# Performance work log

Measured on AMD Instinct MI355X. Metric: run time of the kernel, lower is better.

The kernel has to match this reference:

```python
import jax, jax.numpy as jnp
import numpy as np

N, E, IN, OUT, T = 50000, 800000, 16, 16, 8
LN_EPS = 1e-5


def setup_inputs() -> dict:
    key = jax.random.key(0)
    ks = jax.random.split(key, 8)
    x = jax.random.normal(ks[0], (N, IN), dtype=jnp.float32)
    edge_index = jax.random.randint(ks[1], (2, E), 0, N, dtype=jnp.int64)
    edge_attr = jax.random.normal(ks[2], (E, T), dtype=jnp.float32)
    # LayerNorm params
    ln_gamma = jnp.ones((IN,), dtype=jnp.float32)
    ln_beta = jnp.zeros((IN,), dtype=jnp.float32)
    # edge_nn: Linear(t, in*out)
    w_edge = jax.random.normal(ks[3], (T, IN * OUT), dtype=jnp.float32) * (1.0 / np.sqrt(T))
    b_edge = jax.random.normal(ks[4], (IN * OUT,), dtype=jnp.float32) * 0.01
    # NNConv root weight [in, out] and bias [out]
    root = jax.random.normal(ks[5], (IN, OUT), dtype=jnp.float32) * (1.0 / np.sqrt(IN))
    bias = jax.random.normal(ks[6], (OUT,), dtype=jnp.float32) * 0.01
    return {"x": x, "edge_index": edge_index, "edge_attr": edge_attr,
            "ln_gamma": ln_gamma, "ln_beta": ln_beta,
            "w_edge": w_edge, "b_edge": b_edge, "root": root, "bias": bias}


def reference(x, edge_index, edge_attr, ln_gamma, ln_beta, w_edge, b_edge, root, bias):
    # pre: LayerNorm -> ReLU (Dropout is identity in eval mode)
    mu = jnp.mean(x, axis=-1, keepdims=True)
    var = jnp.mean((x - mu) ** 2, axis=-1, keepdims=True)
    h = (x - mu) * jax.lax.rsqrt(var + LN_EPS) * ln_gamma + ln_beta
    h = jax.nn.relu(h)  # [N, IN]

    # edge MLP -> per-edge weight matrices [E, IN, OUT]
    theta = (edge_attr @ w_edge + b_edge).reshape(E, IN, OUT)

    src = edge_index[0]  # message source j
    dst = edge_index[1]  # aggregation target i (PyG source_to_target flow)

    # per-edge matmul: x_j [E, IN] x theta [E, IN, OUT] -> [E, OUT]
    msg = jnp.einsum('ei,eio->eo', h[src], theta)

    # scatter-add into target nodes
    agg = jax.ops.segment_sum(msg, dst, num_segments=N)  # [N, OUT]

    # root transform + bias
    out = agg + h @ root + bias
    return out
```

## Files before the change

### kernel.cpp

```cpp
#include <hip/hip_runtime.h>

#define N_NODES 50000
#define E_EDGES 800000
#define NTILES  (E_EDGES / 16)

typedef __attribute__((ext_vector_type(8))) short short8;
typedef __attribute__((ext_vector_type(4))) float floatx4;

__device__ __forceinline__ short f2bf(float x) {
    union { float f; unsigned u; } v; v.f = x;
    unsigned r = v.u + 0x7FFFu + ((v.u >> 16) & 1u);
    return (short)(r >> 16);
}

__device__ __forceinline__ unsigned pk_bf16(float lo, float hi) {
    union { float f; unsigned u; } a, b; a.f = lo; b.f = hi;
    return __builtin_amdgcn_perm(b.u, a.u, 0x07060302u);
}

__global__ __launch_bounds__(256) void node_kernel(
    const float* __restrict__ x, const float* __restrict__ gamma,
    const float* __restrict__ beta, const float* __restrict__ root,
    const float* __restrict__ bias, float* __restrict__ h,
    float* __restrict__ out)
{
    int n = blockIdx.x * blockDim.x + threadIdx.x;
    if (n >= N_NODES) return;
    const float* xr = x + n * 16;
    float xv[16];
    #pragma unroll
    for (int i = 0; i < 4; ++i) ((floatx4*)xv)[i] = ((const floatx4*)xr)[i];
    float mu = 0.f;
    #pragma unroll
    for (int i = 0; i < 16; ++i) mu += xv[i];
    mu *= (1.f / 16.f);
    float var = 0.f;
    #pragma unroll
    for (int i = 0; i < 16; ++i) { float d = xv[i] - mu; var += d * d; }
    var *= (1.f / 16.f);
    float rs = rsqrtf(var + 1e-5f);
    float hv[16];
    #pragma unroll
    for (int i = 0; i < 16; ++i) {
        float t = (xv[i] - mu) * rs * gamma[i] + beta[i];
        hv[i] = t > 0.f ? t : 0.f;
    }
    float* hr = h + n * 16;
    #pragma unroll
    for (int i = 0; i < 4; ++i) ((floatx4*)hr)[i] = ((floatx4*)hv)[i];
    float ov[16];
    #pragma unroll
    for (int o = 0; o < 16; ++o) ov[o] = bias[o];
    #pragma unroll
    for (int i = 0; i < 16; ++i) {
        float hi = hv[i];
        #pragma unroll
        for (int o = 0; o < 16; ++o) ov[o] += hi * root[i * 16 + o];
    }
    float* orow = out + n * 16;
    #pragma unroll
    for (int i = 0; i < 4; ++i) ((floatx4*)orow)[i] = ((floatx4*)ov)[i];
}

__global__ __launch_bounds__(256) void prep_kernel(
    const float* __restrict__ w_edge, const float* __restrict__ b_edge,
    short* __restrict__ w2t)
{
    int t = blockIdx.x * blockDim.x + threadIdx.x;
    if (t >= 16 * 160) return;
    int m = t / 160, k = t % 160;
    float v = 0.f;
    if (k < 128)      v = w_edge[(k >> 4) * 256 + (k & 15) * 16 + m];
    else if (k < 144) v = b_edge[(k - 128) * 16 + m];
    w2t[m * 160 + k] = f2bf(v);
}

__global__ __launch_bounds__(256) void edge_kernel(
    const int* __restrict__ eidx, const float* __restrict__ ea,
    const short* __restrict__ w2t, const float* __restrict__ h,
    float* __restrict__ out)
{
    const int lane = threadIdx.x & 63;
    const int wid  = threadIdx.x >> 6;
    const int m = lane & 15;
    const int q = lane >> 4;

    const int tile = blockIdx.x * 4 + wid;
    if (tile >= NTILES) return;

    const int e   = tile * 16 + m;
    const int src = eidx[e];
    const int dst = eidx[E_EDGES + e];

    const short* wp = w2t + m * 160 + 8 * q;
    short8 bfrag[5];
    #pragma unroll
    for (int c = 0; c < 5; ++c)
        bfrag[c] = *(const short8*)(wp + 32 * c);

    const float* er = ea + (size_t)e * 8;
    floatx4 ea0 = ((const floatx4*)er)[0];
    floatx4 ea1 = ((const floatx4*)er)[1];

    const float* hr = h + src * 16 + 8 * (q & 1);
    floatx4 h0 = ((const floatx4*)hr)[0];
    floatx4 h1 = ((const floatx4*)hr)[1];
    float hh[8] = {h0.x, h0.y, h0.z, h0.w, h1.x, h1.y, h1.z, h1.w};

    floatx4 acc = {0.f, 0.f, 0.f, 0.f};
    const int hi_t = q >> 1;
    #pragma unroll
    for (int c = 0; c < 4; ++c) {
        float t_even, t_odd;
        if (c == 0)      { t_even = ea0.x; t_odd = ea0.y; }
        else if (c == 1) { t_even = ea0.z; t_odd = ea0.w; }
        else if (c == 2) { t_even = ea1.x; t_odd = ea1.y; }
        else             { t_even = ea1.z; t_odd = ea1.w; }
        float s = hi_t ? t_odd : t_even;
        union { short8 s8; unsigned u[4]; } af;
        #pragma unroll
        for (int p = 0; p < 4; ++p)
            af.u[p] = pk_bf16(s * hh[2 * p], s * hh[2 * p + 1]);
        acc = __builtin_amdgcn_mfma_f32_16x16x32_bf16(af.s8, bfrag[c], acc, 0, 0, 0);
    }
    {
        const unsigned msk = (q < 2) ? 0xFFFFFFFFu : 0u;
        union { short8 s8; unsigned u[4]; } af;
        #pragma unroll
        for (int p = 0; p < 4; ++p)
            af.u[p] = pk_bf16(hh[2 * p], hh[2 * p + 1]) & msk;
        acc = __builtin_amdgcn_mfma_f32_16x16x32_bf16(af.s8, bfrag[4], acc, 0, 0, 0);
    }

    #pragma unroll
    for (int r = 0; r < 4; ++r) {
        int dr = __shfl(dst, 4 * q + r, 64);
        atomicAdd(out + (size_t)dr * 16 + m, acc[r]);
    }
}

extern "C" void kernel_launch(void* const* d_in, const int* in_sizes, int n_in,
                              void* d_out, int out_size, void* d_ws, size_t ws_size,
                              hipStream_t stream) {
    const float* x        = (const float*)d_in[0];
    const int*   eidx     = (const int*)d_in[1];
    const float* ea       = (const float*)d_in[2];
    const float* ln_gamma = (const float*)d_in[3];
    const float* ln_beta  = (const float*)d_in[4];
    const float* w_edge   = (const float*)d_in[5];
    const float* b_edge   = (const float*)d_in[6];
    const float* root     = (const float*)d_in[7];
    const float* bias     = (const float*)d_in[8];
    float* out = (float*)d_out;

    char* ws = (char*)d_ws;
    float* h   = (float*)ws;
    short* w2t = (short*)(ws + (size_t)N_NODES * 16 * 4);

    prep_kernel<<<10, 256, 0, stream>>>(w_edge, b_edge, w2t);
    node_kernel<<<(N_NODES + 255) / 256, 256, 0, stream>>>(
        x, ln_gamma, ln_beta, root, bias, h, out);
    edge_kernel<<<(NTILES + 3) / 4, 256, 0, stream>>>(eidx, ea, w2t, h, out);
}
```

Baseline: 133.2 us.

## Scatter edge messages as packed fp16 atomics into a half buffer, then merge

Edge messages are now accumulated into a separate fp16 aggregation buffer using packed half2 atomic adds. Lane pairs combine adjacent output columns through a shuffle, which halves the number of atomic operations and the bytes each atomic touches. The node kernel zeroes the buffer, and a new merge kernel adds it into the fp32 output. This trades fewer and narrower atomics for an extra kernel launch and accumulation in fp16, which risks precision loss when many edges sum into one node.

```diff
diff --git a/kernel.cpp b/kernel.cpp
--- a/kernel.cpp
+++ b/kernel.cpp
@@ -1,4 +1,5 @@
 #include <hip/hip_runtime.h>
+#include <hip/hip_fp16.h>
 
 #define N_NODES 50000
 #define E_EDGES 800000
@@ -22,7 +23,7 @@
     const float* __restrict__ x, const float* __restrict__ gamma,
     const float* __restrict__ beta, const float* __restrict__ root,
     const float* __restrict__ bias, float* __restrict__ h,
-    float* __restrict__ out)
+    float* __restrict__ out, __half* __restrict__ agg)
 {
     int n = blockIdx.x * blockDim.x + threadIdx.x;
     if (n >= N_NODES) return;
@@ -48,6 +49,11 @@
     float* hr = h + n * 16;
     #pragma unroll
     for (int i = 0; i < 4; ++i) ((floatx4*)hr)[i] = ((floatx4*)hv)[i];
+
+    floatx4 z = {0.f, 0.f, 0.f, 0.f};
+    floatx4* az = (floatx4*)(agg + (size_t)n * 16);
+    az[0] = z; az[1] = z;
+
     float ov[16];
     #pragma unroll
     for (int o = 0; o < 16; ++o) ov[o] = bias[o];
@@ -78,7 +84,7 @@
 __global__ __launch_bounds__(256) void edge_kernel(
     const int* __restrict__ eidx, const float* __restrict__ ea,
     const short* __restrict__ w2t, const float* __restrict__ h,
-    float* __restrict__ out)
+    __half* __restrict__ agg)
 {
     const int lane = threadIdx.x & 63;
     const int wid  = threadIdx.x >> 6;
@@ -132,11 +138,38 @@
         acc = __builtin_amdgcn_mfma_f32_16x16x32_bf16(af.s8, bfrag[4], acc, 0, 0, 0);
     }
 
+    const int odd = m & 1;
+    const int mlo = m & ~1;
     #pragma unroll
     for (int r = 0; r < 4; ++r) {
+        float p  = __shfl_xor(acc[r], 1, 64);
+        float lo = odd ? p : acc[r];
+        float hi = odd ? acc[r] : p;
+        __half2 v = __floats2half2_rn(lo, hi);
         int dr = __shfl(dst, 4 * q + r, 64);
-        atomicAdd(out + (size_t)dr * 16 + m, acc[r]);
+        if ((r >> 1) == odd)
+            unsafeAtomicAdd((__half2*)(agg + (size_t)dr * 16 + mlo), v);
     }
+}
+
+__global__ __launch_bounds__(256) void merge_kernel(
+    const __half* __restrict__ agg, float* __restrict__ out)
+{
+    int n = blockIdx.x * blockDim.x + threadIdx.x;
+    if (n >= N_NODES) return;
+    const __half2* ar = (const __half2*)(agg + (size_t)n * 16);
+    float* orow = out + (size_t)n * 16;
+    floatx4 o[4];
+    #pragma unroll
+    for (int i = 0; i < 4; ++i) o[i] = ((floatx4*)orow)[i];
+    #pragma unroll
+    for (int j = 0; j < 8; ++j) {
+        float2 f = __half22float2(ar[j]);
+        o[j / 2][(j & 1) * 2 + 0] += f.x;
+        o[j / 2][(j & 1) * 2 + 1] += f.y;
+    }
+    #pragma unroll
+    for (int i = 0; i < 4; ++i) ((floatx4*)orow)[i] = o[i];
 }
 
 extern "C" void kernel_launch(void* const* d_in, const int* in_sizes, int n_in,
@@ -154,11 +187,13 @@
     float* out = (float*)d_out;
 
     char* ws = (char*)d_ws;
-    float* h   = (float*)ws;
-    short* w2t = (short*)(ws + (size_t)N_NODES * 16 * 4);
+    float*  h   = (float*)ws;
+    short*  w2t = (short*)(ws + (size_t)N_NODES * 16 * 4);
+    __half* agg = (__half*)(ws + (size_t)N_NODES * 16 * 4 + 16 * 160 * 2);
 
     prep_kernel<<<10, 256, 0, stream>>>(w_edge, b_edge, w2t);
     node_kernel<<<(N_NODES + 255) / 256, 256, 0, stream>>>(
-        x, ln_gamma, ln_beta, root, bias, h, out);
-    edge_kernel<<<(NTILES + 3) / 4, 256, 0, stream>>>(eidx, ea, w2t, h, out);
+        x, ln_gamma, ln_beta, root, bias, h, out, agg);
+    edge_kernel<<<(NTILES + 3) / 4, 256, 0, stream>>>(eidx, ea, w2t, h, agg);
+    merge_kernel<<<(N_NODES + 255) / 256, 256, 0, stream>>>(agg, out);
 }
```

Result: slower. 136.0 us (+2.1%).

## Replace atomic scatter-add with CSR build and per-node gather aggregation

Applied to the files above, without the earlier changes.

Instead of 12.8M float atomics into the output, the edge kernel writes per-edge messages in fp16 to a buffer. A histogram, three-pass scan and atomic scatter then build a destination-sorted permutation, and a per-node kernel gathers and sums each node's messages. This removes contended float atomics but adds six extra launches, integer atomics, a message buffer round trip and fp16 rounding of messages. Summation order within a node becomes nondeterministic because the permutation is built with atomics.

```diff
diff --git a/kernel.cpp b/kernel.cpp
--- a/kernel.cpp
+++ b/kernel.cpp
@@ -1,8 +1,11 @@
 #include <hip/hip_runtime.h>
+#include <hip/hip_fp16.h>
 
 #define N_NODES 50000
 #define E_EDGES 800000
 #define NTILES  (E_EDGES / 16)
+#define NB_NODE ((N_NODES + 255) / 256)
+#define NB_EDGE ((E_EDGES + 255) / 256)
 
 typedef __attribute__((ext_vector_type(8))) short short8;
 typedef __attribute__((ext_vector_type(4))) float floatx4;
@@ -22,10 +25,11 @@
     const float* __restrict__ x, const float* __restrict__ gamma,
     const float* __restrict__ beta, const float* __restrict__ root,
     const float* __restrict__ bias, float* __restrict__ h,
-    float* __restrict__ out)
+    float* __restrict__ out, int* __restrict__ cnt)
 {
     int n = blockIdx.x * blockDim.x + threadIdx.x;
     if (n >= N_NODES) return;
+    cnt[n] = 0;
     const float* xr = x + n * 16;
     float xv[16];
     #pragma unroll
@@ -48,6 +52,7 @@
     float* hr = h + n * 16;
     #pragma unroll
     for (int i = 0; i < 4; ++i) ((floatx4*)hr)[i] = ((floatx4*)hv)[i];
+
     float ov[16];
     #pragma unroll
     for (int o = 0; o < 16; ++o) ov[o] = bias[o];
@@ -75,22 +80,93 @@
     w2t[m * 160 + k] = f2bf(v);
 }
 
+
+__global__ __launch_bounds__(256) void hist_kernel(
+    const int* __restrict__ eidx, int* __restrict__ cnt)
+{
+    int e = blockIdx.x * 256 + threadIdx.x;
+    if (e < E_EDGES) atomicAdd(cnt + eidx[E_EDGES + e], 1);
+}
+
+__global__ __launch_bounds__(256) void scanA_kernel(
+    const int* __restrict__ cnt, int* __restrict__ tmp, int* __restrict__ part)
+{
+    int i = blockIdx.x * 256 + threadIdx.x;
+    int v = (i < N_NODES) ? cnt[i] : 0;
+    int lane = threadIdx.x & 63, wv = threadIdx.x >> 6;
+    int s = v;
+    #pragma unroll
+    for (int d = 1; d < 64; d <<= 1) { int t = __shfl_up(s, d, 64); if (lane >= d) s += t; }
+    __shared__ int wsum[4];
+    if (lane == 63) wsum[wv] = s;
+    __syncthreads();
+    int base = 0;
+    #pragma unroll
+    for (int w = 0; w < 3; ++w) if (w < wv) base += wsum[w];
+    int incl = s + base;
+    if (i < N_NODES) tmp[i] = incl;
+    if (threadIdx.x == 255) part[blockIdx.x] = incl;
+}
+
+__global__ __launch_bounds__(256) void scanB_kernel(
+    const int* __restrict__ part, int* __restrict__ partoffs)
+{
+    int i = threadIdx.x;
+    int v = (i < NB_NODE) ? part[i] : 0;
+    int lane = threadIdx.x & 63, wv = threadIdx.x >> 6;
+    int s = v;
+    #pragma unroll
+    for (int d = 1; d < 64; d <<= 1) { int t = __shfl_up(s, d, 64); if (lane >= d) s += t; }
+    __shared__ int wsum[4];
+    if (lane == 63) wsum[wv] = s;
+    __syncthreads();
+    int base = 0;
+    #pragma unroll
+    for (int w = 0; w < 3; ++w) if (w < wv) base += wsum[w];
+    if (i < NB_NODE) partoffs[i] = s + base - v;
+}
+
+__global__ __launch_bounds__(256) void scanC_kernel(
+    const int* __restrict__ tmp, const int* __restrict__ cnt,
+    const int* __restrict__ partoffs, int* __restrict__ offs, int* __restrict__ cur)
+{
+    int i = blockIdx.x * 256 + threadIdx.x;
+    if (i < N_NODES) {
+        int o = tmp[i] - cnt[i] + partoffs[blockIdx.x];
+        offs[i] = o;
+        cur[i]  = o;
+    }
+    if (i == 0) offs[N_NODES] = E_EDGES;
+}
+
+__global__ __launch_bounds__(256) void scatter_kernel(
+    const int* __restrict__ eidx, int* __restrict__ cur, int* __restrict__ perm)
+{
+    int e = blockIdx.x * 256 + threadIdx.x;
+    if (e < E_EDGES) {
+        int d = eidx[E_EDGES + e];
+        int pos = atomicAdd(cur + d, 1);
+        perm[pos] = e;
+    }
+}
+
 __global__ __launch_bounds__(256) void edge_kernel(
     const int* __restrict__ eidx, const float* __restrict__ ea,
     const short* __restrict__ w2t, const float* __restrict__ h,
-    float* __restrict__ out)
+    __half* __restrict__ msg)
 {
     const int lane = threadIdx.x & 63;
     const int wid  = threadIdx.x >> 6;
     const int m = lane & 15;
     const int q = lane >> 4;
+    const int odd = m & 1;
+    const int mlo = m & ~1;
 
     const int tile = blockIdx.x * 4 + wid;
     if (tile >= NTILES) return;
 
     const int e   = tile * 16 + m;
     const int src = eidx[e];
-    const int dst = eidx[E_EDGES + e];
 
     const short* wp = w2t + m * 160 + 8 * q;
     short8 bfrag[5];
@@ -111,12 +187,12 @@
     const int hi_t = q >> 1;
     #pragma unroll
     for (int c = 0; c < 4; ++c) {
-        float t_even, t_odd;
-        if (c == 0)      { t_even = ea0.x; t_odd = ea0.y; }
-        else if (c == 1) { t_even = ea0.z; t_odd = ea0.w; }
-        else if (c == 2) { t_even = ea1.x; t_odd = ea1.y; }
-        else             { t_even = ea1.z; t_odd = ea1.w; }
-        float s = hi_t ? t_odd : t_even;
+        float te, to;
+        if (c == 0)      { te = ea0.x; to = ea0.y; }
+        else if (c == 1) { te = ea0.z; to = ea0.w; }
+        else if (c == 2) { te = ea1.x; to = ea1.y; }
+        else             { te = ea1.z; to = ea1.w; }
+        float s = hi_t ? to : te;
         union { short8 s8; unsigned u[4]; } af;
         #pragma unroll
         for (int p = 0; p < 4; ++p)
@@ -132,10 +208,51 @@
         acc = __builtin_amdgcn_mfma_f32_16x16x32_bf16(af.s8, bfrag[4], acc, 0, 0, 0);
     }
 
-    #pragma unroll
-    for (int r = 0; r < 4; ++r) {
-        int dr = __shfl(dst, 4 * q + r, 64);
-        atomicAdd(out + (size_t)dr * 16 + m, acc[r]);
+    float px[4];
+    #pragma unroll
+    for (int r = 0; r < 4; ++r)
+        px[r] = __shfl_xor(acc[r], 1, 64);
+    #pragma unroll
+    for (int k = 0; k < 2; ++k) {
+        const int r = 2 * odd + k;
+        float lo = odd ? px[r] : acc[r];
+        float hi = odd ? acc[r] : px[r];
+        __half2 v = __floats2half2_rn(lo, hi);
+        const int row = 4 * q + 2 * odd + k;
+        *(__half2*)(msg + ((size_t)(tile * 16 + row)) * 16 + mlo) = v;
+    }
+}
+
+__global__ __launch_bounds__(256) void agg_kernel(
+    const int* __restrict__ offs, const int* __restrict__ perm,
+    const __half* __restrict__ msg, float* __restrict__ out)
+{
+    int n = blockIdx.x * 256 + threadIdx.x;
+    if (n >= N_NODES) return;
+    int j0 = offs[n], j1 = offs[n + 1];
+    float s[16];
+    #pragma unroll
+    for (int c = 0; c < 16; ++c) s[c] = 0.f;
+    for (int j = j0; j < j1; ++j) {
+        int e = perm[j];
+        union { floatx4 f4; __half2 h2[4]; } a, b;
+        const floatx4* mr = (const floatx4*)(msg + (size_t)e * 16);
+        a.f4 = mr[0];
+        b.f4 = mr[1];
+        #pragma unroll
+        for (int p = 0; p < 4; ++p) {
+            float2 fa = __half22float2(a.h2[p]);
+            float2 fb = __half22float2(b.h2[p]);
+            s[2 * p]     += fa.x; s[2 * p + 1]     += fa.y;
+            s[8 + 2 * p] += fb.x; s[8 + 2 * p + 1] += fb.y;
+        }
+    }
+    float* orow = out + (size_t)n * 16;
+    #pragma unroll
+    for (int i = 0; i < 4; ++i) {
+        floatx4 o = ((floatx4*)orow)[i];
+        o.x += s[4 * i]; o.y += s[4 * i + 1]; o.z += s[4 * i + 2]; o.w += s[4 * i + 3];
+        ((floatx4*)orow)[i] = o;
     }
 }
 
@@ -153,12 +270,26 @@
     const float* bias     = (const float*)d_in[8];
     float* out = (float*)d_out;
 
-    char* ws = (char*)d_ws;
-    float* h   = (float*)ws;
-    short* w2t = (short*)(ws + (size_t)N_NODES * 16 * 4);
+    char* p = (char*)d_ws;
+    float* h    = (float*)p;  p += (size_t)N_NODES * 16 * 4;
+    short* w2t  = (short*)p;  p += 16 * 160 * 2;
+    int* cnt    = (int*)p;    p += (size_t)N_NODES * 4;
+    int* offs   = (int*)p;    p += (size_t)(N_NODES + 4) * 4;
+    int* cur    = (int*)p;    p += (size_t)N_NODES * 4;
+    int* tmp    = (int*)p;    p += (size_t)N_NODES * 4;
+    int* part   = (int*)p;    p += 256 * 4;
+    int* poffs  = (int*)p;    p += 256 * 4;
+    int* perm   = (int*)p;    p += (size_t)E_EDGES * 4;
+    __half* msg = (__half*)p;
 
     prep_kernel<<<10, 256, 0, stream>>>(w_edge, b_edge, w2t);
-    node_kernel<<<(N_NODES + 255) / 256, 256, 0, stream>>>(
-        x, ln_gamma, ln_beta, root, bias, h, out);
-    edge_kernel<<<(NTILES + 3) / 4, 256, 0, stream>>>(eidx, ea, w2t, h, out);
-}
+    node_kernel<<<NB_NODE, 256, 0, stream>>>(
+        x, ln_gamma, ln_beta, root, bias, h, out, cnt);
+    hist_kernel<<<NB_EDGE, 256, 0, stream>>>(eidx, cnt);
+    scanA_kernel<<<NB_NODE, 256, 0, stream>>>(cnt, tmp, part);
+    scanB_kernel<<<1, 256, 0, stream>>>(part, poffs);
+    scanC_kernel<<<NB_NODE, 256, 0, stream>>>(tmp, cnt, poffs, offs, cur);
+    scatter_kernel<<<NB_EDGE, 256, 0, stream>>>(eidx, cur, perm);
+    edge_kernel<<<(NTILES + 3) / 4, 256, 0, stream>>>(eidx, ea, w2t, h, msg);
+    agg_kernel<<<NB_NODE, 256, 0, stream>>>(offs, perm, msg, out);
+}
```

Result: slower. 236.6 us (+77.6%).

## Privatize scatter-add into 8 partial buffers and reduce in a separate kernel

Applied to the files above, without the earlier changes.

Edge-kernel atomics now go to one of eight per-block-parity copies of the output instead of a single output array, and use unsafeAtomicAdd (hardware float atomics). A new reduce kernel sums the partial copies into the output, which already holds the root transform. The aim is to cut atomic contention on the shared output and use faster atomic instructions. In exchange it adds a memset of about 25 MB, a larger working set that may fit the cache less well, and an extra reduction pass over all partials.

```diff
diff --git a/kernel.cpp b/kernel.cpp
--- a/kernel.cpp
+++ b/kernel.cpp
@@ -3,6 +3,7 @@
 #define N_NODES 50000
 #define E_EDGES 800000
 #define NTILES  (E_EDGES / 16)
+#define NPART   8
 
 typedef __attribute__((ext_vector_type(8))) short short8;
 typedef __attribute__((ext_vector_type(4))) float floatx4;
@@ -48,6 +49,7 @@
     float* hr = h + n * 16;
     #pragma unroll
     for (int i = 0; i < 4; ++i) ((floatx4*)hr)[i] = ((floatx4*)hv)[i];
+
     float ov[16];
     #pragma unroll
     for (int o = 0; o < 16; ++o) ov[o] = bias[o];
@@ -78,7 +80,7 @@
 __global__ __launch_bounds__(256) void edge_kernel(
     const int* __restrict__ eidx, const float* __restrict__ ea,
     const short* __restrict__ w2t, const float* __restrict__ h,
-    float* __restrict__ out)
+    float* __restrict__ partials)
 {
     const int lane = threadIdx.x & 63;
     const int wid  = threadIdx.x >> 6;
@@ -111,12 +113,12 @@
     const int hi_t = q >> 1;
     #pragma unroll
     for (int c = 0; c < 4; ++c) {
-        float t_even, t_odd;
-        if (c == 0)      { t_even = ea0.x; t_odd = ea0.y; }
-        else if (c == 1) { t_even = ea0.z; t_odd = ea0.w; }
-        else if (c == 2) { t_even = ea1.x; t_odd = ea1.y; }
-        else             { t_even = ea1.z; t_odd = ea1.w; }
-        float s = hi_t ? t_odd : t_even;
+        float te, to;
+        if (c == 0)      { te = ea0.x; to = ea0.y; }
+        else if (c == 1) { te = ea0.z; to = ea0.w; }
+        else if (c == 2) { te = ea1.x; to = ea1.y; }
+        else             { te = ea1.z; to = ea1.w; }
+        float s = hi_t ? to : te;
         union { short8 s8; unsigned u[4]; } af;
         #pragma unroll
         for (int p = 0; p < 4; ++p)
@@ -132,11 +134,26 @@
         acc = __builtin_amdgcn_mfma_f32_16x16x32_bf16(af.s8, bfrag[4], acc, 0, 0, 0);
     }
 
+    float* part = partials + (size_t)(blockIdx.x & (NPART - 1)) * N_NODES * 16;
     #pragma unroll
     for (int r = 0; r < 4; ++r) {
         int dr = __shfl(dst, 4 * q + r, 64);
-        atomicAdd(out + (size_t)dr * 16 + m, acc[r]);
+        unsafeAtomicAdd(part + (size_t)dr * 16 + m, acc[r]);
     }
+}
+
+__global__ __launch_bounds__(256) void reduce_kernel(
+    const float* __restrict__ partials, float* __restrict__ out)
+{
+    int t = blockIdx.x * 256 + threadIdx.x;
+    if (t >= N_NODES * 4) return;
+    floatx4 s = ((floatx4*)out)[t];
+    #pragma unroll
+    for (int p = 0; p < NPART; ++p) {
+        floatx4 v = ((const floatx4*)(partials + (size_t)p * N_NODES * 16))[t];
+        s.x += v.x; s.y += v.y; s.z += v.z; s.w += v.w;
+    }
+    ((floatx4*)out)[t] = s;
 }
 
 extern "C" void kernel_launch(void* const* d_in, const int* in_sizes, int n_in,
@@ -153,12 +170,15 @@
     const float* bias     = (const float*)d_in[8];
     float* out = (float*)d_out;
 
-    char* ws = (char*)d_ws;
-    float* h   = (float*)ws;
-    short* w2t = (short*)(ws + (size_t)N_NODES * 16 * 4);
+    char* p = (char*)d_ws;
+    float* h        = (float*)p;  p += (size_t)N_NODES * 16 * 4;
+    short* w2t      = (short*)p;  p += 16 * 160 * 2;
+    float* partials = (float*)p;
 
+    hipMemsetAsync(partials, 0, (size_t)NPART * N_NODES * 16 * 4, stream);
     prep_kernel<<<10, 256, 0, stream>>>(w_edge, b_edge, w2t);
     node_kernel<<<(N_NODES + 255) / 256, 256, 0, stream>>>(
         x, ln_gamma, ln_beta, root, bias, h, out);
-    edge_kernel<<<(NTILES + 3) / 4, 256, 0, stream>>>(eidx, ea, w2t, h, out);
+    edge_kernel<<<(NTILES + 3) / 4, 256, 0, stream>>>(eidx, ea, w2t, h, partials);
+    reduce_kernel<<<(N_NODES * 4 + 255) / 256, 256, 0, stream>>>(partials, out);
 }
```

New measurement: 148.1 us. 1.11x slower.
